# Optimization experiments

Measured on AMD Instinct MI355X. Metric: run time of the kernel, lower is better.

## Reference

```python
import jax, jax.numpy as jnp
import numpy as np

N_NODES = 50000

def setup_inputs() -> dict:
    key = jax.random.key(0)
    k1, k2, k3, k4, k5, k6 = jax.random.split(key, 6)
    N, E, D_IN, D_OUT = N_NODES, 800000, 128, 128
    feature = jax.random.normal(k1, (N, D_IN), dtype=jnp.float32)
    src = jax.random.randint(k2, (E,), 0, N, dtype=jnp.int64)
    dst = jax.random.randint(k3, (E,), 0, N, dtype=jnp.int64)
    w = jax.random.uniform(k4, (E,), dtype=jnp.float32)
    W = jax.random.normal(k5, (D_OUT, D_IN), dtype=jnp.float32) * (1.0 / np.sqrt(D_IN))
    b = jax.random.normal(k6, (D_OUT,), dtype=jnp.float32) * 0.01
    return {"feature": feature, "src": src, "dst": dst, "w": w, "W": W, "b": b}

def reference(feature, src, dst, w, W, b):
    # gcn_msg: gather source node features, scale by per-edge weight  [E, D]
    msg = feature[src] * w[:, None]
    # fn.sum: scatter-sum messages into destination nodes  [N, D]
    agg = jax.ops.segment_sum(msg, dst, num_segments=N_NODES)
    # NodeApplyModule: linear + activation
    h = agg @ W.T + b
    return jax.nn.relu(h)
```

## Files before the change

kernel.cpp:

```cpp
#include <hip/hip_runtime.h>

#define D 128
#define TILE_M 64
#define BS_STRIDE 129
#define AS_STRIDE 68
#define WS_STRIDE 136
#define DS_STRIDE 136
#define GEMM_BLOCKS 768
#define CAP 64
#define CSH 9
#define CBCAP 16384
#define P1_BLOCKS 512
#define P1_CHUNK 1564

typedef __attribute__((ext_vector_type(8))) short short8;
typedef __attribute__((ext_vector_type(4))) float floatx4;
typedef __attribute__((ext_vector_type(4))) unsigned short ushortx4;

__device__ __forceinline__ unsigned short f2bf(float f) {
    unsigned u = __float_as_uint(f);
    u += 0x7fffu + ((u >> 16) & 1u);
    return (unsigned short)(u >> 16);
}

__global__ __launch_bounds__(256) void edge_partition(
    const int* __restrict__ src, const int* __restrict__ dst,
    const float* __restrict__ w, int* __restrict__ gcnt,
    uint2* __restrict__ binned, int N, int E)
{
    __shared__ int hist[128], startb[128], cursor[128], gbase[128];
    __shared__ uint2 grouped[P1_CHUNK];
    const int tid = threadIdx.x;
    const int ncb = (N + 511) >> CSH;
    const int base = blockIdx.x * P1_CHUNK;
    int lim = E - base;
    if (lim > P1_CHUNK) lim = P1_CHUNK;
    if (lim < 0) lim = 0;
    const int lim4 = lim & ~3;

    if (tid < 128) hist[tid] = 0;
    __syncthreads();
    for (int i = tid * 4; i < lim4; i += 1024) {
        const int4 d4 = *reinterpret_cast<const int4*>(dst + base + i);
        atomicAdd(&hist[d4.x >> CSH], 1);
        atomicAdd(&hist[d4.y >> CSH], 1);
        atomicAdd(&hist[d4.z >> CSH], 1);
        atomicAdd(&hist[d4.w >> CSH], 1);
    }
    for (int i = lim4 + tid; i < lim; i += 256)
        atomicAdd(&hist[dst[base + i] >> CSH], 1);
    __syncthreads();
    if (tid == 0) {
        int s = 0;
        for (int b = 0; b < ncb; ++b) { startb[b] = s; s += hist[b]; }
    }
    __syncthreads();
    if (tid < ncb) {
        gbase[tid]  = atomicAdd(&gcnt[tid], hist[tid]);
        cursor[tid] = startb[tid];
    }
    __syncthreads();
    for (int i = tid * 4; i < lim4; i += 1024) {
        const int4   d4 = *reinterpret_cast<const int4*>(dst + base + i);
        const int4   s4 = *reinterpret_cast<const int4*>(src + base + i);
        const float4 w4 = *reinterpret_cast<const float4*>(w + base + i);
#pragma unroll
        for (int j = 0; j < 4; ++j) {
            int   d  = (j == 0) ? d4.x : (j == 1) ? d4.y : (j == 2) ? d4.z : d4.w;
            int   sj = (j == 0) ? s4.x : (j == 1) ? s4.y : (j == 2) ? s4.z : s4.w;
            float wj = (j == 0) ? w4.x : (j == 1) ? w4.y : (j == 2) ? w4.z : w4.w;
            unsigned rec = ((unsigned)f2bf(wj) << 16) | (unsigned)sj;
            int g = atomicAdd(&cursor[d >> CSH], 1);
            grouped[g] = make_uint2((unsigned)d, rec);
        }
    }
    for (int i = lim4 + tid; i < lim; i += 256) {
        int e = base + i;
        int d = dst[e];
        unsigned rec = ((unsigned)f2bf(w[e]) << 16) | (unsigned)src[e];
        int g = atomicAdd(&cursor[d >> CSH], 1);
        grouped[g] = make_uint2((unsigned)d, rec);
    }
    __syncthreads();
    for (int i = tid; i < lim; i += 256) {
        uint2 v = grouped[i];
        int b = (int)(v.x >> CSH);
        int off = gbase[b] + (i - startb[b]);
        if (off < CBCAP)
            binned[(size_t)b * CBCAP + (size_t)off] = v;
    }
}

__global__ __launch_bounds__(256) void csr_gemm(
    const uint2* __restrict__ binned, const int* __restrict__ gcnt,
    unsigned* __restrict__ ep, int* __restrict__ cnt,
    const float* __restrict__ feat, const float* __restrict__ Wm,
    unsigned short* __restrict__ tf, int N)
{
    __shared__ char smem[52224] __attribute__((aligned(16)));
    const int tid = threadIdx.x;
    const int nfb = (N + 127) >> 7;

    if ((int)blockIdx.x < nfb) {
        unsigned* rowsT = reinterpret_cast<unsigned*>(smem);
        int* lcnt       = reinterpret_cast<int*>(smem + 32768);
        int* maxcp      = reinterpret_cast<int*>(smem + 32768 + 512);
        const int fb = blockIdx.x;
        const int d0 = fb << 7;
        const int cb = fb >> 2;

        if (tid < 128) lcnt[tid] = 0;
        __syncthreads();
        int len = gcnt[cb];
        len = len < CBCAP ? len : CBCAP;
        const uint2* bp = binned + (size_t)cb * CBCAP;
        const int len2 = len & ~1;
        for (int i = tid * 2; i < len2; i += 512) {
            const uint4 v2 = *reinterpret_cast<const uint4*>(bp + i);
            int da = (int)v2.x;
            if ((da >> 7) == fb) {
                int pos = atomicAdd(&lcnt[da & 127], 1);
                if (pos < CAP) rowsT[pos * 128 + (da & 127)] = v2.y;
            }
            int db = (int)v2.z;
            if ((db >> 7) == fb) {
                int pos = atomicAdd(&lcnt[db & 127], 1);
                if (pos < CAP) rowsT[pos * 128 + (db & 127)] = v2.w;
            }
        }
        for (int i = len2 + tid; i < len; i += 256) {
            uint2 v = bp[i];
            int d = (int)v.x;
            if ((d >> 7) == fb) {
                int pos = atomicAdd(&lcnt[d & 127], 1);
                if (pos < CAP) rowsT[pos * 128 + (d & 127)] = v.y;
            }
        }
        __syncthreads();
        if (tid == 0) {
            int m = 0;
            for (int j = 0; j < 128; ++j) m = m > lcnt[j] ? m : lcnt[j];
            *maxcp = m < CAP ? m : CAP;
        }
        __syncthreads();
        const int pu = *maxcp;
        for (int idx = tid; idx < (pu << 7); idx += 256) {
            int p = idx >> 7, j = idx & 127;
            int d = d0 + j;
            if (d < N) ep[(size_t)p * N + d] = rowsT[idx];
        }
        if (tid < 128) {
            int d = d0 + tid;
            if (d < N) cnt[d] = lcnt[tid];
        }
        return;
    }

    unsigned short* Ws = reinterpret_cast<unsigned short*>(smem);
    unsigned short* Ds = reinterpret_cast<unsigned short*>(smem + 34816);

    for (int idx = tid; idx < 128 * 128 / 4; idx += 256) {
        int r = idx >> 5;
        int c = (idx & 31) * 4;
        const float4 v = reinterpret_cast<const float4*>(Wm)[idx];
        ushortx4 s;
        s[0] = f2bf(v.x); s[1] = f2bf(v.y); s[2] = f2bf(v.z); s[3] = f2bf(v.w);
        *reinterpret_cast<ushortx4*>(&Ws[r * WS_STRIDE + c]) = s;
    }
    __syncthreads();

    const int lane = tid & 63;
    const int wave = tid >> 6;
    const int kq = (lane >> 4) * 8;
    const int ntiles = (N + 63) >> 6;

    for (int t = blockIdx.x - nfb; t < ntiles; t += GEMM_BLOCKS) {
        const int node0 = t * 64;
        const int mr = node0 + wave * 16 + (lane & 15);
        const float* arow = feat + (size_t)(mr < N ? mr : (N - 1)) * D + kq;

        short8 a[4];
#pragma unroll
        for (int kt = 0; kt < 4; ++kt) {
            const float* p = arow + kt * 32;
            const float4 lo = *reinterpret_cast<const float4*>(p);
            const float4 hi = *reinterpret_cast<const float4*>(p + 4);
            short8 v;
            v[0] = (short)f2bf(lo.x); v[1] = (short)f2bf(lo.y);
            v[2] = (short)f2bf(lo.z); v[3] = (short)f2bf(lo.w);
            v[4] = (short)f2bf(hi.x); v[5] = (short)f2bf(hi.y);
            v[6] = (short)f2bf(hi.z); v[7] = (short)f2bf(hi.w);
            a[kt] = v;
        }

        floatx4 acc[8];
#pragma unroll
        for (int nt = 0; nt < 8; ++nt) {
            acc[nt][0] = 0.f; acc[nt][1] = 0.f; acc[nt][2] = 0.f; acc[nt][3] = 0.f;
        }
#pragma unroll
        for (int nt = 0; nt < 8; ++nt) {
            const unsigned short* brow = &Ws[(nt * 16 + (lane & 15)) * WS_STRIDE + kq];
#pragma unroll
            for (int kt = 0; kt < 4; ++kt) {
                short8 b = *reinterpret_cast<const short8*>(brow + kt * 32);
                acc[nt] = __builtin_amdgcn_mfma_f32_16x16x32_bf16(a[kt], b, acc[nt], 0, 0, 0);
            }
        }

        __syncthreads();
        const int mlocal = wave * 16 + (lane >> 4) * 4;
        const int col = lane & 15;
#pragma unroll
        for (int r = 0; r < 4; ++r) {
            unsigned short* drow = &Ds[(mlocal + r) * DS_STRIDE + col];
#pragma unroll
            for (int nt = 0; nt < 8; ++nt)
                drow[nt * 16] = f2bf(acc[nt][r]);
        }
        __syncthreads();

        for (int idx = tid; idx < 64 * 16; idx += 256) {
            int row = idx >> 4;
            int chunk = idx & 15;
            int m = node0 + row;
            if (m < N) {
                uint4 v = *reinterpret_cast<const uint4*>(&Ds[row * DS_STRIDE + chunk * 8]);
                *reinterpret_cast<uint4*>(tf + (size_t)m * D + chunk * 8) = v;
            }
        }
    }
}

__global__ __launch_bounds__(256) void csr_gather_bf16(
    const unsigned short* __restrict__ tf, const unsigned* __restrict__ ep,
    const int* __restrict__ cnt, const float* __restrict__ bias,
    float* __restrict__ out, int N)
{
    int node = blockIdx.x * 16 + (threadIdx.x >> 4);
    if (node >= N) return;
    const int lane = threadIdx.x & 15;
    const int c = lane << 3;
    const unsigned* col = ep + node;
    int end = cnt[node];
    end = end < CAP ? end : CAP;
    int p = 0;
    float a0 = 0.f, a1 = 0.f, a2 = 0.f, a3 = 0.f;
    float a4 = 0.f, a5 = 0.f, a6 = 0.f, a7 = 0.f;

#define ACC8(Q, W)                                       \
    a0 += __uint_as_float((Q).x << 16) * (W);            \
    a1 += __uint_as_float((Q).x & 0xffff0000u) * (W);    \
    a2 += __uint_as_float((Q).y << 16) * (W);            \
    a3 += __uint_as_float((Q).y & 0xffff0000u) * (W);    \
    a4 += __uint_as_float((Q).z << 16) * (W);            \
    a5 += __uint_as_float((Q).z & 0xffff0000u) * (W);    \
    a6 += __uint_as_float((Q).w << 16) * (W);            \
    a7 += __uint_as_float((Q).w & 0xffff0000u) * (W);

    for (; p + 7 < end; p += 8) {
        unsigned r[8];
#pragma unroll
        for (int j = 0; j < 8; ++j) r[j] = col[(size_t)(p + j) * N];
        uint4 q[8];
        float wv[8];
#pragma unroll
        for (int j = 0; j < 8; ++j) {
            q[j] = *reinterpret_cast<const uint4*>(tf + (size_t)(r[j] & 0xffffu) * D + c);
            wv[j] = __uint_as_float(r[j] & 0xffff0000u);
        }
#pragma unroll
        for (int j = 0; j < 8; ++j) { ACC8(q[j], wv[j]) }
    }
    for (; p + 3 < end; p += 4) {
        unsigned r[4];
#pragma unroll
        for (int j = 0; j < 4; ++j) r[j] = col[(size_t)(p + j) * N];
        uint4 q[4];
        float wv[4];
#pragma unroll
        for (int j = 0; j < 4; ++j) {
            q[j] = *reinterpret_cast<const uint4*>(tf + (size_t)(r[j] & 0xffffu) * D + c);
            wv[j] = __uint_as_float(r[j] & 0xffff0000u);
        }
#pragma unroll
        for (int j = 0; j < 4; ++j) { ACC8(q[j], wv[j]) }
    }
    for (; p < end; ++p) {
        unsigned r = col[(size_t)p * N];
        float wv = __uint_as_float(r & 0xffff0000u);
        uint4 q = *reinterpret_cast<const uint4*>(tf + (size_t)(r & 0xffffu) * D + c);
        ACC8(q, wv)
    }
#undef ACC8

    const float4 bv0 = *reinterpret_cast<const float4*>(bias + c);
    const float4 bv1 = *reinterpret_cast<const float4*>(bias + c + 4);
    float4 r0, r1;
    r0.x = fmaxf(a0 + bv0.x, 0.f);
    r0.y = fmaxf(a1 + bv0.y, 0.f);
    r0.z = fmaxf(a2 + bv0.z, 0.f);
    r0.w = fmaxf(a3 + bv0.w, 0.f);
    r1.x = fmaxf(a4 + bv1.x, 0.f);
    r1.y = fmaxf(a5 + bv1.y, 0.f);
    r1.z = fmaxf(a6 + bv1.z, 0.f);
    r1.w = fmaxf(a7 + bv1.w, 0.f);
    float* o = out + (size_t)node * D + c;
    *reinterpret_cast<float4*>(o) = r0;
    *reinterpret_cast<float4*>(o + 4) = r1;
}

__global__ __launch_bounds__(256) void edge_scatter(
    const float* __restrict__ feat, const int* __restrict__ src,
    const int* __restrict__ dst, const float* __restrict__ w,
    float* __restrict__ agg, int E)
{
    long long idx = (long long)blockIdx.x * 256 + threadIdx.x;
    int e = (int)(idx >> 5);
    if (e >= E) return;
    int c = ((int)idx & 31) << 2;
    int s = src[e];
    int d = dst[e];
    float wv = w[e];
    const float4 f = *reinterpret_cast<const float4*>(feat + (size_t)s * D + c);
    float* a = agg + (size_t)d * D + c;
    atomicAdd(a + 0, f.x * wv);
    atomicAdd(a + 1, f.y * wv);
    atomicAdd(a + 2, f.z * wv);
    atomicAdd(a + 3, f.w * wv);
}

__global__ __launch_bounds__(256) void node_linear(
    const float* __restrict__ in, const float* __restrict__ Wm,
    const float* __restrict__ bias, float* __restrict__ out, int N)
{
    __shared__ float Bs[64 * BS_STRIDE];
    __shared__ float As[TILE_M * AS_STRIDE];
    const int tid = threadIdx.x;
    const int tx = tid & 15;
    const int ty = tid >> 4;
    const int node0 = blockIdx.x * TILE_M;
    float acc[4][8];
#pragma unroll
    for (int i = 0; i < 4; ++i)
#pragma unroll
        for (int jj = 0; jj < 8; ++jj) acc[i][jj] = 0.0f;
    for (int kh = 0; kh < 2; ++kh) {
        const int kbase = kh * 64;
        for (int i = tid; i < 128 * 64; i += 256) {
            int j = i >> 6, k = i & 63;
            Bs[k * BS_STRIDE + j] = Wm[j * 128 + kbase + k];
        }
        for (int i = tid; i < TILE_M * 64; i += 256) {
            int m = i >> 6, k = i & 63;
            int n = node0 + m;
            As[m * AS_STRIDE + k] = (n < N) ? in[(size_t)n * D + kbase + k] : 0.0f;
        }
        __syncthreads();
        for (int k0 = 0; k0 < 64; k0 += 4) {
            float a[4][4];
#pragma unroll
            for (int i = 0; i < 4; ++i) {
                const float4 v = *reinterpret_cast<const float4*>(&As[(ty * 4 + i) * AS_STRIDE + k0]);
                a[i][0] = v.x; a[i][1] = v.y; a[i][2] = v.z; a[i][3] = v.w;
            }
#pragma unroll
            for (int kk = 0; kk < 4; ++kk) {
                float bv[8];
#pragma unroll
                for (int jj = 0; jj < 8; ++jj) bv[jj] = Bs[(k0 + kk) * BS_STRIDE + tx + 16 * jj];
#pragma unroll
                for (int i = 0; i < 4; ++i)
#pragma unroll
                    for (int jj = 0; jj < 8; ++jj) acc[i][jj] += a[i][kk] * bv[jj];
            }
        }
        __syncthreads();
    }
    float bv[8];
#pragma unroll
    for (int jj = 0; jj < 8; ++jj) bv[jj] = bias[tx + 16 * jj];
#pragma unroll
    for (int i = 0; i < 4; ++i) {
        int n = node0 + ty * 4 + i;
        if (n < N) {
            float* o = out + (size_t)n * D;
#pragma unroll
            for (int jj = 0; jj < 8; ++jj) {
                float v = acc[i][jj] + bv[jj];
                o[tx + 16 * jj] = v > 0.0f ? v : 0.0f;
            }
        }
    }
}

extern "C" void kernel_launch(void* const* d_in, const int* in_sizes, int n_in,
                              void* d_out, int out_size, void* d_ws, size_t ws_size,
                              hipStream_t stream) {
    const float* feat = (const float*)d_in[0];
    const int*   src  = (const int*)d_in[1];
    const int*   dst  = (const int*)d_in[2];
    const float* w    = (const float*)d_in[3];
    const float* Wm   = (const float*)d_in[4];
    const float* bias = (const float*)d_in[5];
    float* out = (float*)d_out;

    const int N = in_sizes[0] / D;
    const int E = in_sizes[1];

    const int ncb = (N + 511) >> CSH;
    const int nfb = (N + 127) >> 7;

    const size_t ep_b     = (size_t)N * CAP * 4;
    const size_t cnt_b    = (size_t)N * sizeof(int);
    const size_t tf_b     = (size_t)N * D * 2;
    const size_t binned_b = (size_t)ncb * CBCAP * sizeof(uint2);
    const size_t gcnt_b   = 128 * sizeof(int);
    auto align_up = [](size_t x) { return (x + 255) & ~(size_t)255; };

    const size_t need_full = align_up(ep_b) + align_up(cnt_b) + align_up(tf_b) +
                             align_up(binned_b) + align_up(gcnt_b);

    if (ws_size >= need_full && N <= 65536 &&
        E <= P1_BLOCKS * P1_CHUNK &&
        (long long)E <= (long long)N * (CAP / 4)) {
        char* p = (char*)d_ws;
        unsigned* ep     = (unsigned*)p;       p += align_up(ep_b);
        int*      cnt    = (int*)p;            p += align_up(cnt_b);
        unsigned short* tf = (unsigned short*)p; p += align_up(tf_b);
        uint2*    binned = (uint2*)p;          p += align_up(binned_b);
        int*      gcnt   = (int*)p;

        (void)hipMemsetAsync(gcnt, 0, gcnt_b, stream);
        edge_partition<<<P1_BLOCKS, 256, 0, stream>>>(src, dst, w, gcnt, binned, N, E);
        csr_gemm<<<nfb + GEMM_BLOCKS, 256, 0, stream>>>(binned, gcnt, ep, cnt,
                                                        feat, Wm, tf, N);
        csr_gather_bf16<<<(N + 15) / 16, 256, 0, stream>>>(tf, ep, cnt, bias, out, N);
    } else {
        (void)hipMemsetAsync(out, 0, (size_t)N * D * sizeof(float), stream);
        long long st = (long long)E * 32;
        edge_scatter<<<(int)((st + 255) / 256), 256, 0, stream>>>(feat, src, dst, w, out, E);
        node_linear<<<(N + TILE_M - 1) / TILE_M, 256, 0, stream>>>(out, Wm, bias, out, N);
    }
}
```

Before: 147.5 us.

## Fuse partition, CSR build, GEMM and gather into one cooperative persistent kernel

Replaces the three-kernel pipeline with a single cooperative kernel of 768 persistent blocks. Stages are separated by grid.sync(): edge partitioning over smaller chunks, then CSR bin building plus GEMM tiles handed out dynamically through an atomic tile counter, then the gather. The aim is to cut kernel launch gaps and tail effects between stages and to balance GEMM work dynamically. The cost is grid-wide barriers, occupancy limits from needing all blocks co-resident, and more partition chunks (smaller P1_CHUNK). It falls back to the separate kernels if the cooperative launch fails.

```diff
diff --git a/kernel.cpp b/kernel.cpp
--- a/kernel.cpp
+++ b/kernel.cpp
@@ -1,4 +1,7 @@
 #include <hip/hip_runtime.h>
+#include <hip/hip_cooperative_groups.h>
+
+namespace cg = cooperative_groups;
 
 #define D 128
 #define TILE_M 64
@@ -6,12 +9,12 @@
 #define AS_STRIDE 68
 #define WS_STRIDE 136
 #define DS_STRIDE 136
+#define MEGA_BLOCKS 768
 #define GEMM_BLOCKS 768
 #define CAP 64
 #define CSH 9
 #define CBCAP 16384
-#define P1_BLOCKS 512
-#define P1_CHUNK 1564
+#define P1_CHUNK 1044
 
 typedef __attribute__((ext_vector_type(8))) short short8;
 typedef __attribute__((ext_vector_type(4))) float floatx4;
@@ -23,16 +26,20 @@
     return (unsigned short)(u >> 16);
 }
 
-__global__ __launch_bounds__(256) void edge_partition(
-    const int* __restrict__ src, const int* __restrict__ dst,
+
+__device__ __forceinline__ void partition_chunk(
+    char* smem, const int* __restrict__ src, const int* __restrict__ dst,
     const float* __restrict__ w, int* __restrict__ gcnt,
-    uint2* __restrict__ binned, int N, int E)
-{
-    __shared__ int hist[128], startb[128], cursor[128], gbase[128];
-    __shared__ uint2 grouped[P1_CHUNK];
+    uint2* __restrict__ binned, int N, int E, int cidx)
+{
+    int* hist      = reinterpret_cast<int*>(smem);
+    int* startb    = reinterpret_cast<int*>(smem + 512);
+    int* cursor    = reinterpret_cast<int*>(smem + 1024);
+    int* gbase     = reinterpret_cast<int*>(smem + 1536);
+    uint2* grouped = reinterpret_cast<uint2*>(smem + 2048);
     const int tid = threadIdx.x;
     const int ncb = (N + 511) >> CSH;
-    const int base = blockIdx.x * P1_CHUNK;
+    const int base = cidx * P1_CHUNK;
     int lim = E - base;
     if (lim > P1_CHUNK) lim = P1_CHUNK;
     if (lim < 0) lim = 0;
@@ -89,77 +96,71 @@
         if (off < CBCAP)
             binned[(size_t)b * CBCAP + (size_t)off] = v;
     }
-}
-
-__global__ __launch_bounds__(256) void csr_gemm(
-    const uint2* __restrict__ binned, const int* __restrict__ gcnt,
-    unsigned* __restrict__ ep, int* __restrict__ cnt,
-    const float* __restrict__ feat, const float* __restrict__ Wm,
-    unsigned short* __restrict__ tf, int N)
-{
-    __shared__ char smem[52224] __attribute__((aligned(16)));
+    __syncthreads();
+}
+
+__device__ __forceinline__ void csr_build_bin(
+    char* smem, const uint2* __restrict__ binned, const int* __restrict__ gcnt,
+    unsigned* __restrict__ ep, int* __restrict__ cnt, int N, int fb)
+{
+    unsigned* rowsT = reinterpret_cast<unsigned*>(smem);
+    int* lcnt       = reinterpret_cast<int*>(smem + 32768);
+    int* maxcp      = reinterpret_cast<int*>(smem + 32768 + 512);
     const int tid = threadIdx.x;
-    const int nfb = (N + 127) >> 7;
-
-    if ((int)blockIdx.x < nfb) {
-        unsigned* rowsT = reinterpret_cast<unsigned*>(smem);
-        int* lcnt       = reinterpret_cast<int*>(smem + 32768);
-        int* maxcp      = reinterpret_cast<int*>(smem + 32768 + 512);
-        const int fb = blockIdx.x;
-        const int d0 = fb << 7;
-        const int cb = fb >> 2;
-
-        if (tid < 128) lcnt[tid] = 0;
-        __syncthreads();
-        int len = gcnt[cb];
-        len = len < CBCAP ? len : CBCAP;
-        const uint2* bp = binned + (size_t)cb * CBCAP;
-        const int len2 = len & ~1;
-        for (int i = tid * 2; i < len2; i += 512) {
-            const uint4 v2 = *reinterpret_cast<const uint4*>(bp + i);
-            int da = (int)v2.x;
-            if ((da >> 7) == fb) {
-                int pos = atomicAdd(&lcnt[da & 127], 1);
-                if (pos < CAP) rowsT[pos * 128 + (da & 127)] = v2.y;
-            }
-            int db = (int)v2.z;
-            if ((db >> 7) == fb) {
-                int pos = atomicAdd(&lcnt[db & 127], 1);
-                if (pos < CAP) rowsT[pos * 128 + (db & 127)] = v2.w;
-            }
-        }
-        for (int i = len2 + tid; i < len; i += 256) {
-            uint2 v = bp[i];
-            int d = (int)v.x;
-            if ((d >> 7) == fb) {
-                int pos = atomicAdd(&lcnt[d & 127], 1);
-                if (pos < CAP) rowsT[pos * 128 + (d & 127)] = v.y;
-            }
-        }
-        __syncthreads();
-        if (tid == 0) {
-            int m = 0;
-            for (int j = 0; j < 128; ++j) m = m > lcnt[j] ? m : lcnt[j];
-            *maxcp = m < CAP ? m : CAP;
-        }
-        __syncthreads();
-        const int pu = *maxcp;
-        for (int idx = tid; idx < (pu << 7); idx += 256) {
-            int p = idx >> 7, j = idx & 127;
-            int d = d0 + j;
-            if (d < N) ep[(size_t)p * N + d] = rowsT[idx];
-        }
-        if (tid < 128) {
-            int d = d0 + tid;
-            if (d < N) cnt[d] = lcnt[tid];
-        }
-        return;
-    }
-
+    const int d0 = fb << 7;
+    const int cb = fb >> 2;
+
+    if (tid < 128) lcnt[tid] = 0;
+    __syncthreads();
+    int len = gcnt[cb];
+    len = len < CBCAP ? len : CBCAP;
+    const uint2* bp = binned + (size_t)cb * CBCAP;
+    const int len2 = len & ~1;
+    for (int i = tid * 2; i < len2; i += 512) {
+        const uint4 v2 = *reinterpret_cast<const uint4*>(bp + i);
+        int da = (int)v2.x;
+        if ((da >> 7) == fb) {
+            int pos = atomicAdd(&lcnt[da & 127], 1);
+            if (pos < CAP) rowsT[pos * 128 + (da & 127)] = v2.y;
+        }
+        int db = (int)v2.z;
+        if ((db >> 7) == fb) {
+            int pos = atomicAdd(&lcnt[db & 127], 1);
+            if (pos < CAP) rowsT[pos * 128 + (db & 127)] = v2.w;
+        }
+    }
+    for (int i = len2 + tid; i < len; i += 256) {
+        uint2 v = bp[i];
+        int d = (int)v.x;
+        if ((d >> 7) == fb) {
+            int pos = atomicAdd(&lcnt[d & 127], 1);
+            if (pos < CAP) rowsT[pos * 128 + (d & 127)] = v.y;
+        }
+    }
+    __syncthreads();
+    if (tid == 0) {
+        int m = 0;
+        for (int j = 0; j < 128; ++j) m = m > lcnt[j] ? m : lcnt[j];
+        *maxcp = m < CAP ? m : CAP;
+    }
+    __syncthreads();
+    const int pu = *maxcp;
+    for (int idx = tid; idx < (pu << 7); idx += 256) {
+        int p = idx >> 7, j = idx & 127;
+        int d = d0 + j;
+        if (d < N) ep[(size_t)p * N + d] = rowsT[idx];
+    }
+    if (tid < 128) {
+        int d = d0 + tid;
+        if (d < N) cnt[d] = lcnt[tid];
+    }
+    __syncthreads();
+}
+
+__device__ __forceinline__ void gemm_stage_W(char* smem, const float* __restrict__ Wm)
+{
     unsigned short* Ws = reinterpret_cast<unsigned short*>(smem);
-    unsigned short* Ds = reinterpret_cast<unsigned short*>(smem + 34816);
-
-    for (int idx = tid; idx < 128 * 128 / 4; idx += 256) {
+    for (int idx = threadIdx.x; idx < 128 * 128 / 4; idx += 256) {
         int r = idx >> 5;
         int c = (idx & 31) * 4;
         const float4 v = reinterpret_cast<const float4*>(Wm)[idx];
@@ -168,76 +169,80 @@
         *reinterpret_cast<ushortx4*>(&Ws[r * WS_STRIDE + c]) = s;
     }
     __syncthreads();
-
+}
+
+__device__ __forceinline__ void gemm_tile(
+    char* smem, const float* __restrict__ feat,
+    unsigned short* __restrict__ tf, int N, int t)
+{
+    unsigned short* Ws = reinterpret_cast<unsigned short*>(smem);
+    unsigned short* Ds = reinterpret_cast<unsigned short*>(smem + 34816);
+    const int tid = threadIdx.x;
     const int lane = tid & 63;
     const int wave = tid >> 6;
     const int kq = (lane >> 4) * 8;
-    const int ntiles = (N + 63) >> 6;
-
-    for (int t = blockIdx.x - nfb; t < ntiles; t += GEMM_BLOCKS) {
-        const int node0 = t * 64;
-        const int mr = node0 + wave * 16 + (lane & 15);
-        const float* arow = feat + (size_t)(mr < N ? mr : (N - 1)) * D + kq;
-
-        short8 a[4];
+    const int node0 = t * 64;
+    const int mr = node0 + wave * 16 + (lane & 15);
+    const float* arow = feat + (size_t)(mr < N ? mr : (N - 1)) * D + kq;
+
+    short8 a[4];
+#pragma unroll
+    for (int kt = 0; kt < 4; ++kt) {
+        const float* p = arow + kt * 32;
+        const float4 lo = *reinterpret_cast<const float4*>(p);
+        const float4 hi = *reinterpret_cast<const float4*>(p + 4);
+        short8 v;
+        v[0] = (short)f2bf(lo.x); v[1] = (short)f2bf(lo.y);
+        v[2] = (short)f2bf(lo.z); v[3] = (short)f2bf(lo.w);
+        v[4] = (short)f2bf(hi.x); v[5] = (short)f2bf(hi.y);
+        v[6] = (short)f2bf(hi.z); v[7] = (short)f2bf(hi.w);
+        a[kt] = v;
+    }
+
+    floatx4 acc[8];
+#pragma unroll
+    for (int nt = 0; nt < 8; ++nt) {
+        acc[nt][0] = 0.f; acc[nt][1] = 0.f; acc[nt][2] = 0.f; acc[nt][3] = 0.f;
+    }
+#pragma unroll
+    for (int nt = 0; nt < 8; ++nt) {
+        const unsigned short* brow = &Ws[(nt * 16 + (lane & 15)) * WS_STRIDE + kq];
 #pragma unroll
         for (int kt = 0; kt < 4; ++kt) {
-            const float* p = arow + kt * 32;
-            const float4 lo = *reinterpret_cast<const float4*>(p);
-            const float4 hi = *reinterpret_cast<const float4*>(p + 4);
-            short8 v;
-            v[0] = (short)f2bf(lo.x); v[1] = (short)f2bf(lo.y);
-            v[2] = (short)f2bf(lo.z); v[3] = (short)f2bf(lo.w);
-            v[4] = (short)f2bf(hi.x); v[5] = (short)f2bf(hi.y);
-            v[6] = (short)f2bf(hi.z); v[7] = (short)f2bf(hi.w);
-            a[kt] = v;
-        }
-
-        floatx4 acc[8];
-#pragma unroll
-        for (int nt = 0; nt < 8; ++nt) {
-            acc[nt][0] = 0.f; acc[nt][1] = 0.f; acc[nt][2] = 0.f; acc[nt][3] = 0.f;
-        }
-#pragma unroll
-        for (int nt = 0; nt < 8; ++nt) {
-            const unsigned short* brow = &Ws[(nt * 16 + (lane & 15)) * WS_STRIDE + kq];
-#pragma unroll
-            for (int kt = 0; kt < 4; ++kt) {
-                short8 b = *reinterpret_cast<const short8*>(brow + kt * 32);
-                acc[nt] = __builtin_amdgcn_mfma_f32_16x16x32_bf16(a[kt], b, acc[nt], 0, 0, 0);
-            }
-        }
-
-        __syncthreads();
-        const int mlocal = wave * 16 + (lane >> 4) * 4;
-        const int col = lane & 15;
-#pragma unroll
-        for (int r = 0; r < 4; ++r) {
-            unsigned short* drow = &Ds[(mlocal + r) * DS_STRIDE + col];
-#pragma unroll
-            for (int nt = 0; nt < 8; ++nt)
-                drow[nt * 16] = f2bf(acc[nt][r]);
-        }
-        __syncthreads();
-
-        for (int idx = tid; idx < 64 * 16; idx += 256) {
-            int row = idx >> 4;
-            int chunk = idx & 15;
-            int m = node0 + row;
-            if (m < N) {
-                uint4 v = *reinterpret_cast<const uint4*>(&Ds[row * DS_STRIDE + chunk * 8]);
-                *reinterpret_cast<uint4*>(tf + (size_t)m * D + chunk * 8) = v;
-            }
-        }
-    }
-}
-
-__global__ __launch_bounds__(256) void csr_gather_bf16(
+            short8 b = *reinterpret_cast<const short8*>(brow + kt * 32);
+            acc[nt] = __builtin_amdgcn_mfma_f32_16x16x32_bf16(a[kt], b, acc[nt], 0, 0, 0);
+        }
+    }
+
+    __syncthreads();
+    const int mlocal = wave * 16 + (lane >> 4) * 4;
+    const int col = lane & 15;
+#pragma unroll
+    for (int r = 0; r < 4; ++r) {
+        unsigned short* drow = &Ds[(mlocal + r) * DS_STRIDE + col];
+#pragma unroll
+        for (int nt = 0; nt < 8; ++nt)
+            drow[nt * 16] = f2bf(acc[nt][r]);
+    }
+    __syncthreads();
+
+    for (int idx = tid; idx < 64 * 16; idx += 256) {
+        int row = idx >> 4;
+        int chunk = idx & 15;
+        int m = node0 + row;
+        if (m < N) {
+            uint4 v = *reinterpret_cast<const uint4*>(&Ds[row * DS_STRIDE + chunk * 8]);
+            *reinterpret_cast<uint4*>(tf + (size_t)m * D + chunk * 8) = v;
+        }
+    }
+}
+
+__device__ __forceinline__ void gather16(
     const unsigned short* __restrict__ tf, const unsigned* __restrict__ ep,
     const int* __restrict__ cnt, const float* __restrict__ bias,
-    float* __restrict__ out, int N)
-{
-    int node = blockIdx.x * 16 + (threadIdx.x >> 4);
+    float* __restrict__ out, int N, int g)
+{
+    int node = g * 16 + (threadIdx.x >> 4);
     if (node >= N) return;
     const int lane = threadIdx.x & 15;
     const int c = lane << 3;
@@ -310,6 +315,80 @@
     *reinterpret_cast<float4*>(o + 4) = r1;
 }
 
+__global__ __launch_bounds__(256) void gcn_mega(
+    const float* __restrict__ feat, const float* __restrict__ Wm,
+    unsigned short* __restrict__ tf,
+    const int* __restrict__ src, const int* __restrict__ dst,
+    const float* __restrict__ w,
+    int* __restrict__ gcnt, uint2* __restrict__ binned,
+    unsigned* __restrict__ ep, int* __restrict__ cnt,
+    int* __restrict__ tcnt,
+    const float* __restrict__ bias, float* __restrict__ out,
+    int N, int E)
+{
+    __shared__ char smem[52224] __attribute__((aligned(16)));
+    __shared__ int tsh;
+    cg::grid_group grid = cg::this_grid();
+    const int nfb = (N + 127) >> 7;
+    const int nchunks = (E + P1_CHUNK - 1) / P1_CHUNK;
+    const int ntiles = (N + 63) >> 6;
+
+    for (int c = blockIdx.x; c < nchunks; c += gridDim.x)
+        partition_chunk(smem, src, dst, w, gcnt, binned, N, E, c);
+    grid.sync();
+
+    if ((int)blockIdx.x < nfb)
+        csr_build_bin(smem, binned, gcnt, ep, cnt, N, blockIdx.x);
+    gemm_stage_W(smem, Wm);
+    for (;;) {
+        if (threadIdx.x == 0) tsh = atomicAdd(tcnt, 1);
+        __syncthreads();
+        int t = tsh;
+        if (t >= ntiles) break;
+        gemm_tile(smem, feat, tf, N, t);
+    }
+    grid.sync();
+
+    const int ngr = (N + 15) >> 4;
+    for (int g = blockIdx.x; g < ngr; g += gridDim.x)
+        gather16(tf, ep, cnt, bias, out, N, g);
+}
+
+__global__ __launch_bounds__(256) void edge_partition(
+    const int* __restrict__ src, const int* __restrict__ dst,
+    const float* __restrict__ w, int* __restrict__ gcnt,
+    uint2* __restrict__ binned, int N, int E)
+{
+    __shared__ char smem[2048 + P1_CHUNK * 8] __attribute__((aligned(16)));
+    partition_chunk(smem, src, dst, w, gcnt, binned, N, E, blockIdx.x);
+}
+
+__global__ __launch_bounds__(256) void csr_gemm(
+    const uint2* __restrict__ binned, const int* __restrict__ gcnt,
+    unsigned* __restrict__ ep, int* __restrict__ cnt,
+    const float* __restrict__ feat, const float* __restrict__ Wm,
+    unsigned short* __restrict__ tf, int N)
+{
+    __shared__ char smem[52224] __attribute__((aligned(16)));
+    const int nfb = (N + 127) >> 7;
+    if ((int)blockIdx.x < nfb) {
+        csr_build_bin(smem, binned, gcnt, ep, cnt, N, blockIdx.x);
+        return;
+    }
+    gemm_stage_W(smem, Wm);
+    const int ntiles = (N + 63) >> 6;
+    for (int t = blockIdx.x - nfb; t < ntiles; t += GEMM_BLOCKS)
+        gemm_tile(smem, feat, tf, N, t);
+}
+
+__global__ __launch_bounds__(256) void csr_gather_bf16(
+    const unsigned short* __restrict__ tf, const unsigned* __restrict__ ep,
+    const int* __restrict__ cnt, const float* __restrict__ bias,
+    float* __restrict__ out, int N)
+{
+    gather16(tf, ep, cnt, bias, out, N, blockIdx.x);
+}
+
 __global__ __launch_bounds__(256) void edge_scatter(
     const float* __restrict__ feat, const int* __restrict__ src,
     const int* __restrict__ dst, const float* __restrict__ w,
@@ -410,19 +489,19 @@
 
     const int ncb = (N + 511) >> CSH;
     const int nfb = (N + 127) >> 7;
+    const int nchunks = (E + P1_CHUNK - 1) / P1_CHUNK;
 
     const size_t ep_b     = (size_t)N * CAP * 4;
     const size_t cnt_b    = (size_t)N * sizeof(int);
     const size_t tf_b     = (size_t)N * D * 2;
     const size_t binned_b = (size_t)ncb * CBCAP * sizeof(uint2);
-    const size_t gcnt_b   = 128 * sizeof(int);
+    const size_t gcnt_b   = 192 * sizeof(int);
     auto align_up = [](size_t x) { return (x + 255) & ~(size_t)255; };
 
     const size_t need_full = align_up(ep_b) + align_up(cnt_b) + align_up(tf_b) +
                              align_up(binned_b) + align_up(gcnt_b);
 
     if (ws_size >= need_full && N <= 65536 &&
-        E <= P1_BLOCKS * P1_CHUNK &&
         (long long)E <= (long long)N * (CAP / 4)) {
         char* p = (char*)d_ws;
         unsigned* ep     = (unsigned*)p;       p += align_up(ep_b);
@@ -430,12 +509,23 @@
         unsigned short* tf = (unsigned short*)p; p += align_up(tf_b);
         uint2*    binned = (uint2*)p;          p += align_up(binned_b);
         int*      gcnt   = (int*)p;
-
-        (void)hipMemsetAsync(gcnt, 0, gcnt_b, stream);
-        edge_partition<<<P1_BLOCKS, 256, 0, stream>>>(src, dst, w, gcnt, binned, N, E);
-        csr_gemm<<<nfb + GEMM_BLOCKS, 256, 0, stream>>>(binned, gcnt, ep, cnt,
-                                                        feat, Wm, tf, N);
-        csr_gather_bf16<<<(N + 15) / 16, 256, 0, stream>>>(tf, ep, cnt, bias, out, N);
+        int*      tcnt   = gcnt + 128;
+
+        (void)hipMemsetAsync(gcnt, 0, 132 * sizeof(int), stream);
+
+        int Nv = N, Ev = E;
+        void* kargs[] = { (void*)&feat, (void*)&Wm, (void*)&tf, (void*)&src,
+                          (void*)&dst, (void*)&w, (void*)&gcnt, (void*)&binned,
+                          (void*)&ep, (void*)&cnt, (void*)&tcnt, (void*)&bias,
+                          (void*)&out, (void*)&Nv, (void*)&Ev };
+        hipError_t err = hipLaunchCooperativeKernel(
+            (const void*)gcn_mega, dim3(MEGA_BLOCKS), dim3(256), kargs, 0, stream);
+        if (err != hipSuccess) {
+            edge_partition<<<nchunks, 256, 0, stream>>>(src, dst, w, gcnt, binned, N, E);
+            csr_gemm<<<nfb + GEMM_BLOCKS, 256, 0, stream>>>(binned, gcnt, ep, cnt,
+                                                            feat, Wm, tf, N);
+            csr_gather_bf16<<<(N + 15) / 16, 256, 0, stream>>>(tf, ep, cnt, bias, out, N);
+        }
     } else {
         (void)hipMemsetAsync(out, 0, (size_t)N * D * sizeof(float), stream);
         long long st = (long long)E * 32;
```

Result: slower. 338.3 us (+129.3%).

## Fuse partition with GEMM and build per-node CSR inside the gather kernel

Applied to the files above, without the earlier changes.

The edge partitioning and the feature×W GEMM now run as independent block sets of one launch, so they can overlap. The separate pass that wrote a transposed CSR (ep/cnt) to global memory is gone: the gather kernel now bins its 64 destination nodes' edges directly into shared memory and accumulates from it. Coarse bins shrink to 256 nodes with a smaller capacity, which cuts the redundant bin scan each gather block does. In exchange, each gather block re-reads its whole coarse bin, and the smaller bin capacity raises the risk of silent overflow truncation on skewed graphs.

```diff
diff --git a/kernel.cpp b/kernel.cpp
--- a/kernel.cpp
+++ b/kernel.cpp
@@ -6,11 +6,11 @@
 #define AS_STRIDE 68
 #define WS_STRIDE 136
 #define DS_STRIDE 136
+#define P1_BLOCKS 512
 #define GEMM_BLOCKS 768
 #define CAP 64
-#define CSH 9
-#define CBCAP 16384
-#define P1_BLOCKS 512
+#define CSH 8
+#define CBCAP 8192
 #define P1_CHUNK 1564
 
 typedef __attribute__((ext_vector_type(8))) short short8;
@@ -23,22 +23,26 @@
     return (unsigned short)(u >> 16);
 }
 
-__global__ __launch_bounds__(256) void edge_partition(
-    const int* __restrict__ src, const int* __restrict__ dst,
+
+__device__ __forceinline__ void partition_chunk(
+    char* smem, const int* __restrict__ src, const int* __restrict__ dst,
     const float* __restrict__ w, int* __restrict__ gcnt,
-    uint2* __restrict__ binned, int N, int E)
-{
-    __shared__ int hist[128], startb[128], cursor[128], gbase[128];
-    __shared__ uint2 grouped[P1_CHUNK];
+    uint2* __restrict__ binned, int N, int E, int cidx)
+{
+    int* hist      = reinterpret_cast<int*>(smem);
+    int* startb    = reinterpret_cast<int*>(smem + 1024);
+    int* cursor    = reinterpret_cast<int*>(smem + 2048);
+    int* gbase     = reinterpret_cast<int*>(smem + 3072);
+    uint2* grouped = reinterpret_cast<uint2*>(smem + 4096);
     const int tid = threadIdx.x;
-    const int ncb = (N + 511) >> CSH;
-    const int base = blockIdx.x * P1_CHUNK;
+    const int ncb = (N + 255) >> CSH;
+    const int base = cidx * P1_CHUNK;
     int lim = E - base;
     if (lim > P1_CHUNK) lim = P1_CHUNK;
     if (lim < 0) lim = 0;
     const int lim4 = lim & ~3;
 
-    if (tid < 128) hist[tid] = 0;
+    hist[tid] = 0;
     __syncthreads();
     for (int i = tid * 4; i < lim4; i += 1024) {
         const int4 d4 = *reinterpret_cast<const int4*>(dst + base + i);
@@ -89,77 +93,13 @@
         if (off < CBCAP)
             binned[(size_t)b * CBCAP + (size_t)off] = v;
     }
-}
-
-__global__ __launch_bounds__(256) void csr_gemm(
-    const uint2* __restrict__ binned, const int* __restrict__ gcnt,
-    unsigned* __restrict__ ep, int* __restrict__ cnt,
-    const float* __restrict__ feat, const float* __restrict__ Wm,
-    unsigned short* __restrict__ tf, int N)
-{
-    __shared__ char smem[52224] __attribute__((aligned(16)));
-    const int tid = threadIdx.x;
-    const int nfb = (N + 127) >> 7;
-
-    if ((int)blockIdx.x < nfb) {
-        unsigned* rowsT = reinterpret_cast<unsigned*>(smem);
-        int* lcnt       = reinterpret_cast<int*>(smem + 32768);
-        int* maxcp      = reinterpret_cast<int*>(smem + 32768 + 512);
-        const int fb = blockIdx.x;
-        const int d0 = fb << 7;
-        const int cb = fb >> 2;
-
-        if (tid < 128) lcnt[tid] = 0;
-        __syncthreads();
-        int len = gcnt[cb];
-        len = len < CBCAP ? len : CBCAP;
-        const uint2* bp = binned + (size_t)cb * CBCAP;
-        const int len2 = len & ~1;
-        for (int i = tid * 2; i < len2; i += 512) {
-            const uint4 v2 = *reinterpret_cast<const uint4*>(bp + i);
-            int da = (int)v2.x;
-            if ((da >> 7) == fb) {
-                int pos = atomicAdd(&lcnt[da & 127], 1);
-                if (pos < CAP) rowsT[pos * 128 + (da & 127)] = v2.y;
-            }
-            int db = (int)v2.z;
-            if ((db >> 7) == fb) {
-                int pos = atomicAdd(&lcnt[db & 127], 1);
-                if (pos < CAP) rowsT[pos * 128 + (db & 127)] = v2.w;
-            }
-        }
-        for (int i = len2 + tid; i < len; i += 256) {
-            uint2 v = bp[i];
-            int d = (int)v.x;
-            if ((d >> 7) == fb) {
-                int pos = atomicAdd(&lcnt[d & 127], 1);
-                if (pos < CAP) rowsT[pos * 128 + (d & 127)] = v.y;
-            }
-        }
-        __syncthreads();
-        if (tid == 0) {
-            int m = 0;
-            for (int j = 0; j < 128; ++j) m = m > lcnt[j] ? m : lcnt[j];
-            *maxcp = m < CAP ? m : CAP;
-        }
-        __syncthreads();
-        const int pu = *maxcp;
-        for (int idx = tid; idx < (pu << 7); idx += 256) {
-            int p = idx >> 7, j = idx & 127;
-            int d = d0 + j;
-            if (d < N) ep[(size_t)p * N + d] = rowsT[idx];
-        }
-        if (tid < 128) {
-            int d = d0 + tid;
-            if (d < N) cnt[d] = lcnt[tid];
-        }
-        return;
-    }
-
+    __syncthreads();
+}
+
+__device__ __forceinline__ void gemm_stage_W(char* smem, const float* __restrict__ Wm)
+{
     unsigned short* Ws = reinterpret_cast<unsigned short*>(smem);
-    unsigned short* Ds = reinterpret_cast<unsigned short*>(smem + 34816);
-
-    for (int idx = tid; idx < 128 * 128 / 4; idx += 256) {
+    for (int idx = threadIdx.x; idx < 128 * 128 / 4; idx += 256) {
         int r = idx >> 5;
         int c = (idx & 31) * 4;
         const float4 v = reinterpret_cast<const float4*>(Wm)[idx];
@@ -168,85 +108,140 @@
         *reinterpret_cast<ushortx4*>(&Ws[r * WS_STRIDE + c]) = s;
     }
     __syncthreads();
-
+}
+
+__device__ __forceinline__ void gemm_tile(
+    char* smem, const float* __restrict__ feat,
+    unsigned short* __restrict__ tf, int N, int t)
+{
+    unsigned short* Ws = reinterpret_cast<unsigned short*>(smem);
+    unsigned short* Ds = reinterpret_cast<unsigned short*>(smem + 34816);
+    const int tid = threadIdx.x;
     const int lane = tid & 63;
     const int wave = tid >> 6;
     const int kq = (lane >> 4) * 8;
+    const int node0 = t * 64;
+    const int mr = node0 + wave * 16 + (lane & 15);
+    const float* arow = feat + (size_t)(mr < N ? mr : (N - 1)) * D + kq;
+
+    short8 a[4];
+#pragma unroll
+    for (int kt = 0; kt < 4; ++kt) {
+        const float* p = arow + kt * 32;
+        const float4 lo = *reinterpret_cast<const float4*>(p);
+        const float4 hi = *reinterpret_cast<const float4*>(p + 4);
+        short8 v;
+        v[0] = (short)f2bf(lo.x); v[1] = (short)f2bf(lo.y);
+        v[2] = (short)f2bf(lo.z); v[3] = (short)f2bf(lo.w);
+        v[4] = (short)f2bf(hi.x); v[5] = (short)f2bf(hi.y);
+        v[6] = (short)f2bf(hi.z); v[7] = (short)f2bf(hi.w);
+        a[kt] = v;
+    }
+
+    floatx4 acc[8];
+#pragma unroll
+    for (int nt = 0; nt < 8; ++nt) {
+        acc[nt][0] = 0.f; acc[nt][1] = 0.f; acc[nt][2] = 0.f; acc[nt][3] = 0.f;
+    }
+#pragma unroll
+    for (int nt = 0; nt < 8; ++nt) {
+        const unsigned short* brow = &Ws[(nt * 16 + (lane & 15)) * WS_STRIDE + kq];
+#pragma unroll
+        for (int kt = 0; kt < 4; ++kt) {
+            short8 b = *reinterpret_cast<const short8*>(brow + kt * 32);
+            acc[nt] = __builtin_amdgcn_mfma_f32_16x16x32_bf16(a[kt], b, acc[nt], 0, 0, 0);
+        }
+    }
+
+    __syncthreads();
+    const int mlocal = wave * 16 + (lane >> 4) * 4;
+    const int col = lane & 15;
+#pragma unroll
+    for (int r = 0; r < 4; ++r) {
+        unsigned short* drow = &Ds[(mlocal + r) * DS_STRIDE + col];
+#pragma unroll
+        for (int nt = 0; nt < 8; ++nt)
+            drow[nt * 16] = f2bf(acc[nt][r]);
+    }
+    __syncthreads();
+
+    for (int idx = tid; idx < 64 * 16; idx += 256) {
+        int row = idx >> 4;
+        int chunk = idx & 15;
+        int m = node0 + row;
+        if (m < N) {
+            uint4 v = *reinterpret_cast<const uint4*>(&Ds[row * DS_STRIDE + chunk * 8]);
+            *reinterpret_cast<uint4*>(tf + (size_t)m * D + chunk * 8) = v;
+        }
+    }
+}
+
+__global__ __launch_bounds__(256) void part_gemm(
+    const int* __restrict__ src, const int* __restrict__ dst,
+    const float* __restrict__ w, int* __restrict__ gcnt,
+    uint2* __restrict__ binned,
+    const float* __restrict__ feat, const float* __restrict__ Wm,
+    unsigned short* __restrict__ tf, int N, int E)
+{
+    __shared__ char smem[52224] __attribute__((aligned(16)));
+    if ((int)blockIdx.x < P1_BLOCKS) {
+        const int nchunks = (E + P1_CHUNK - 1) / P1_CHUNK;
+        for (int ci = blockIdx.x; ci < nchunks; ci += P1_BLOCKS)
+            partition_chunk(smem, src, dst, w, gcnt, binned, N, E, ci);
+        return;
+    }
+    gemm_stage_W(smem, Wm);
     const int ntiles = (N + 63) >> 6;
-
-    for (int t = blockIdx.x - nfb; t < ntiles; t += GEMM_BLOCKS) {
-        const int node0 = t * 64;
-        const int mr = node0 + wave * 16 + (lane & 15);
-        const float* arow = feat + (size_t)(mr < N ? mr : (N - 1)) * D + kq;
-
-        short8 a[4];
-#pragma unroll
-        for (int kt = 0; kt < 4; ++kt) {
-            const float* p = arow + kt * 32;
-            const float4 lo = *reinterpret_cast<const float4*>(p);
-            const float4 hi = *reinterpret_cast<const float4*>(p + 4);
-            short8 v;
-            v[0] = (short)f2bf(lo.x); v[1] = (short)f2bf(lo.y);
-            v[2] = (short)f2bf(lo.z); v[3] = (short)f2bf(lo.w);
-            v[4] = (short)f2bf(hi.x); v[5] = (short)f2bf(hi.y);
-            v[6] = (short)f2bf(hi.z); v[7] = (short)f2bf(hi.w);
-            a[kt] = v;
-        }
-
-        floatx4 acc[8];
-#pragma unroll
-        for (int nt = 0; nt < 8; ++nt) {
-            acc[nt][0] = 0.f; acc[nt][1] = 0.f; acc[nt][2] = 0.f; acc[nt][3] = 0.f;
-        }
-#pragma unroll
-        for (int nt = 0; nt < 8; ++nt) {
-            const unsigned short* brow = &Ws[(nt * 16 + (lane & 15)) * WS_STRIDE + kq];
-#pragma unroll
-            for (int kt = 0; kt < 4; ++kt) {
-                short8 b = *reinterpret_cast<const short8*>(brow + kt * 32);
-                acc[nt] = __builtin_amdgcn_mfma_f32_16x16x32_bf16(a[kt], b, acc[nt], 0, 0, 0);
-            }
-        }
-
-        __syncthreads();
-        const int mlocal = wave * 16 + (lane >> 4) * 4;
-        const int col = lane & 15;
-#pragma unroll
-        for (int r = 0; r < 4; ++r) {
-            unsigned short* drow = &Ds[(mlocal + r) * DS_STRIDE + col];
-#pragma unroll
-            for (int nt = 0; nt < 8; ++nt)
-                drow[nt * 16] = f2bf(acc[nt][r]);
-        }
-        __syncthreads();
-
-        for (int idx = tid; idx < 64 * 16; idx += 256) {
-            int row = idx >> 4;
-            int chunk = idx & 15;
-            int m = node0 + row;
-            if (m < N) {
-                uint4 v = *reinterpret_cast<const uint4*>(&Ds[row * DS_STRIDE + chunk * 8]);
-                *reinterpret_cast<uint4*>(tf + (size_t)m * D + chunk * 8) = v;
-            }
-        }
-    }
-}
-
-__global__ __launch_bounds__(256) void csr_gather_bf16(
-    const unsigned short* __restrict__ tf, const unsigned* __restrict__ ep,
-    const int* __restrict__ cnt, const float* __restrict__ bias,
+    for (int t = blockIdx.x - P1_BLOCKS; t < ntiles; t += GEMM_BLOCKS)
+        gemm_tile(smem, feat, tf, N, t);
+}
+
+__global__ __launch_bounds__(256) void csr_gather_fused(
+    const uint2* __restrict__ binned, const int* __restrict__ gcnt,
+    const unsigned short* __restrict__ tf, const float* __restrict__ bias,
     float* __restrict__ out, int N)
 {
-    int node = blockIdx.x * 16 + (threadIdx.x >> 4);
-    if (node >= N) return;
-    const int lane = threadIdx.x & 15;
+    __shared__ unsigned rowsT[CAP * 64];
+    __shared__ int lcnt[64];
+    const int tid = threadIdx.x;
+    const int fb = blockIdx.x;
+    const int d0 = fb << 6;
+    const int cb = fb >> 2;
+
+    if (tid < 64) lcnt[tid] = 0;
+    __syncthreads();
+    int len = gcnt[cb];
+    len = len < CBCAP ? len : CBCAP;
+    const uint2* bp = binned + (size_t)cb * CBCAP;
+    const int len2 = len & ~1;
+    for (int i = tid * 2; i < len2; i += 512) {
+        const uint4 v2 = *reinterpret_cast<const uint4*>(bp + i);
+        int da = (int)v2.x;
+        if ((da >> 6) == fb) {
+            int pos = atomicAdd(&lcnt[da & 63], 1);
+            if (pos < CAP) rowsT[pos * 64 + (da & 63)] = v2.y;
+        }
+        int db = (int)v2.z;
+        if ((db >> 6) == fb) {
+            int pos = atomicAdd(&lcnt[db & 63], 1);
+            if (pos < CAP) rowsT[pos * 64 + (db & 63)] = v2.w;
+        }
+    }
+    for (int i = len2 + tid; i < len; i += 256) {
+        uint2 v = bp[i];
+        int d = (int)v.x;
+        if ((d >> 6) == fb) {
+            int pos = atomicAdd(&lcnt[d & 63], 1);
+            if (pos < CAP) rowsT[pos * 64 + (d & 63)] = v.y;
+        }
+    }
+    __syncthreads();
+
+    const int g = tid >> 4;
+    const int lane = tid & 15;
     const int c = lane << 3;
-    const unsigned* col = ep + node;
-    int end = cnt[node];
-    end = end < CAP ? end : CAP;
-    int p = 0;
-    float a0 = 0.f, a1 = 0.f, a2 = 0.f, a3 = 0.f;
-    float a4 = 0.f, a5 = 0.f, a6 = 0.f, a7 = 0.f;
+    const float4 bv0 = *reinterpret_cast<const float4*>(bias + c);
+    const float4 bv1 = *reinterpret_cast<const float4*>(bias + c + 4);
 
 #define ACC8(Q, W)                                       \
     a0 += __uint_as_float((Q).x << 16) * (W);            \
@@ -258,56 +253,65 @@
     a6 += __uint_as_float((Q).w << 16) * (W);            \
     a7 += __uint_as_float((Q).w & 0xffff0000u) * (W);
 
-    for (; p + 7 < end; p += 8) {
-        unsigned r[8];
-#pragma unroll
-        for (int j = 0; j < 8; ++j) r[j] = col[(size_t)(p + j) * N];
-        uint4 q[8];
-        float wv[8];
-#pragma unroll
-        for (int j = 0; j < 8; ++j) {
-            q[j] = *reinterpret_cast<const uint4*>(tf + (size_t)(r[j] & 0xffffu) * D + c);
-            wv[j] = __uint_as_float(r[j] & 0xffff0000u);
-        }
-#pragma unroll
-        for (int j = 0; j < 8; ++j) { ACC8(q[j], wv[j]) }
-    }
-    for (; p + 3 < end; p += 4) {
-        unsigned r[4];
-#pragma unroll
-        for (int j = 0; j < 4; ++j) r[j] = col[(size_t)(p + j) * N];
-        uint4 q[4];
-        float wv[4];
-#pragma unroll
-        for (int j = 0; j < 4; ++j) {
-            q[j] = *reinterpret_cast<const uint4*>(tf + (size_t)(r[j] & 0xffffu) * D + c);
-            wv[j] = __uint_as_float(r[j] & 0xffff0000u);
-        }
-#pragma unroll
-        for (int j = 0; j < 4; ++j) { ACC8(q[j], wv[j]) }
-    }
-    for (; p < end; ++p) {
-        unsigned r = col[(size_t)p * N];
-        float wv = __uint_as_float(r & 0xffff0000u);
-        uint4 q = *reinterpret_cast<const uint4*>(tf + (size_t)(r & 0xffffu) * D + c);
-        ACC8(q, wv)
+#pragma unroll
+    for (int it = 0; it < 4; ++it) {
+        const int j = g + (it << 4);
+        const int node = d0 + j;
+        if (node >= N) break;
+        int end = lcnt[j];
+        end = end < CAP ? end : CAP;
+        const unsigned* col = &rowsT[j];
+        float a0 = 0.f, a1 = 0.f, a2 = 0.f, a3 = 0.f;
+        float a4 = 0.f, a5 = 0.f, a6 = 0.f, a7 = 0.f;
+        int p = 0;
+        for (; p + 7 < end; p += 8) {
+            unsigned r[8];
+#pragma unroll
+            for (int k = 0; k < 8; ++k) r[k] = col[(p + k) * 64];
+            uint4 q[8];
+            float wv[8];
+#pragma unroll
+            for (int k = 0; k < 8; ++k) {
+                q[k] = *reinterpret_cast<const uint4*>(tf + (size_t)(r[k] & 0xffffu) * D + c);
+                wv[k] = __uint_as_float(r[k] & 0xffff0000u);
+            }
+#pragma unroll
+            for (int k = 0; k < 8; ++k) { ACC8(q[k], wv[k]) }
+        }
+        for (; p + 3 < end; p += 4) {
+            unsigned r[4];
+#pragma unroll
+            for (int k = 0; k < 4; ++k) r[k] = col[(p + k) * 64];
+            uint4 q[4];
+            float wv[4];
+#pragma unroll
+            for (int k = 0; k < 4; ++k) {
+                q[k] = *reinterpret_cast<const uint4*>(tf + (size_t)(r[k] & 0xffffu) * D + c);
+                wv[k] = __uint_as_float(r[k] & 0xffff0000u);
+            }
+#pragma unroll
+            for (int k = 0; k < 4; ++k) { ACC8(q[k], wv[k]) }
+        }
+        for (; p < end; ++p) {
+            unsigned r = col[p * 64];
+            float wv = __uint_as_float(r & 0xffff0000u);
+            uint4 q = *reinterpret_cast<const uint4*>(tf + (size_t)(r & 0xffffu) * D + c);
+            ACC8(q, wv)
+        }
+        float4 r0, r1;
+        r0.x = fmaxf(a0 + bv0.x, 0.f);
+        r0.y = fmaxf(a1 + bv0.y, 0.f);
+        r0.z = fmaxf(a2 + bv0.z, 0.f);
+        r0.w = fmaxf(a3 + bv0.w, 0.f);
+        r1.x = fmaxf(a4 + bv1.x, 0.f);
+        r1.y = fmaxf(a5 + bv1.y, 0.f);
+        r1.z = fmaxf(a6 + bv1.z, 0.f);
+        r1.w = fmaxf(a7 + bv1.w, 0.f);
+        float* o = out + (size_t)node * D + c;
+        *reinterpret_cast<float4*>(o) = r0;
+        *reinterpret_cast<float4*>(o + 4) = r1;
     }
 #undef ACC8
-
-    const float4 bv0 = *reinterpret_cast<const float4*>(bias + c);
-    const float4 bv1 = *reinterpret_cast<const float4*>(bias + c + 4);
-    float4 r0, r1;
-    r0.x = fmaxf(a0 + bv0.x, 0.f);
-    r0.y = fmaxf(a1 + bv0.y, 0.f);
-    r0.z = fmaxf(a2 + bv0.z, 0.f);
-    r0.w = fmaxf(a3 + bv0.w, 0.f);
-    r1.x = fmaxf(a4 + bv1.x, 0.f);
-    r1.y = fmaxf(a5 + bv1.y, 0.f);
-    r1.z = fmaxf(a6 + bv1.z, 0.f);
-    r1.w = fmaxf(a7 + bv1.w, 0.f);
-    float* o = out + (size_t)node * D + c;
-    *reinterpret_cast<float4*>(o) = r0;
-    *reinterpret_cast<float4*>(o + 4) = r1;
 }
 
 __global__ __launch_bounds__(256) void edge_scatter(
@@ -408,34 +412,27 @@
     const int N = in_sizes[0] / D;
     const int E = in_sizes[1];
 
-    const int ncb = (N + 511) >> CSH;
-    const int nfb = (N + 127) >> 7;
-
-    const size_t ep_b     = (size_t)N * CAP * 4;
-    const size_t cnt_b    = (size_t)N * sizeof(int);
+    const int ncb = (N + 255) >> CSH;
+    const int nfb = (N + 63) >> 6;
+
     const size_t tf_b     = (size_t)N * D * 2;
     const size_t binned_b = (size_t)ncb * CBCAP * sizeof(uint2);
-    const size_t gcnt_b   = 128 * sizeof(int);
+    const size_t gcnt_b   = 256 * sizeof(int);
     auto align_up = [](size_t x) { return (x + 255) & ~(size_t)255; };
 
-    const size_t need_full = align_up(ep_b) + align_up(cnt_b) + align_up(tf_b) +
-                             align_up(binned_b) + align_up(gcnt_b);
+    const size_t need_full = align_up(tf_b) + align_up(binned_b) + align_up(gcnt_b);
 
     if (ws_size >= need_full && N <= 65536 &&
-        E <= P1_BLOCKS * P1_CHUNK &&
         (long long)E <= (long long)N * (CAP / 4)) {
         char* p = (char*)d_ws;
-        unsigned* ep     = (unsigned*)p;       p += align_up(ep_b);
-        int*      cnt    = (int*)p;            p += align_up(cnt_b);
         unsigned short* tf = (unsigned short*)p; p += align_up(tf_b);
-        uint2*    binned = (uint2*)p;          p += align_up(binned_b);
+        uint2*    binned = (uint2*)p;            p += align_up(binned_b);
         int*      gcnt   = (int*)p;
 
         (void)hipMemsetAsync(gcnt, 0, gcnt_b, stream);
-        edge_partition<<<P1_BLOCKS, 256, 0, stream>>>(src, dst, w, gcnt, binned, N, E);
-        csr_gemm<<<nfb + GEMM_BLOCKS, 256, 0, stream>>>(binned, gcnt, ep, cnt,
-                                                        feat, Wm, tf, N);
-        csr_gather_bf16<<<(N + 15) / 16, 256, 0, stream>>>(tf, ep, cnt, bias, out, N);
+        part_gemm<<<P1_BLOCKS + GEMM_BLOCKS, 256, 0, stream>>>(
+            src, dst, w, gcnt, binned, feat, Wm, tf, N, E);
+        csr_gather_fused<<<nfb, 256, 0, stream>>>(binned, gcnt, tf, bias, out, N);
     } else {
         (void)hipMemsetAsync(out, 0, (size_t)N * D * sizeof(float), stream);
         long long st = (long long)E * 32;
```

Measured after the change: 142.2 us. 3.6% less time.
